# Kernel optimization log

Measured on AMD Instinct MI355X. Metric: run time of the kernel, lower is better.

The kernel has to match this reference:

```python
import jax, jax.numpy as jnp
import numpy as np

# irreps_in = 128x0e + 64x1o + 32x2e -> (multiplicity, 2l+1) blocks
IRREPS = [(128, 1), (64, 3), (32, 5)]
DIM = sum(m * d for m, d in IRREPS)  # 480
EPS = 1e-8


def setup_inputs() -> dict:
    key = jax.random.key(0)
    features = jax.random.normal(key, (100000, DIM), dtype=jnp.float32)
    return {"features": features}


def reference(features) -> jnp.ndarray:
    batch = features.shape[:-1]
    out_blocks = []
    off = 0
    for mul, d in IRREPS:  # fixed small structural loop over irrep types
        block = features[..., off:off + mul * d].reshape(*batch, mul, d)
        # per-irrep L2 norm over the (2l+1) components -> (..., mul)
        norms = jnp.sqrt(jnp.sum(block * block, axis=-1))
        eps_norms = jnp.maximum(norms, EPS)
        scalings = jax.nn.silu(eps_norms) / eps_norms
        out_blocks.append((block * scalings[..., None]).reshape(*batch, mul * d))
        off += mul * d
    return jnp.concatenate(out_blocks, axis=-1)
```

## Files before the change

kernel.cpp:

```cpp
#include <hip/hip_runtime.h>
#include <math.h>

#define DIM 480
#define ROWS 8
#define BLOCK 64
#define NLOADS 15

__device__ __forceinline__ float sig_of(float n) {
    n = fmaxf(n, 1e-8f);
    return __builtin_amdgcn_rcpf(1.0f + __expf(-n));
}

template <int R>
__device__ __forceinline__ void scale_groups(float* sbuf, int lane) {
    #pragma unroll
    for (int k = 0; k < R * 2; ++k) {
        const int a = k * 64 + lane;
        float* p = sbuf + (a >> 7) * DIM + (a & 127);
        const float x = *p;
        *p = x * sig_of(fabsf(x));
    }
    #pragma unroll
    for (int k = 0; k < R; ++k) {
        const int b = k * 64 + lane;
        float* p = sbuf + (b >> 6) * DIM + 128 + 3 * (b & 63);
        const float x0 = p[0], x1 = p[1], x2 = p[2];
        const float s = sig_of(sqrtf(x0*x0 + x1*x1 + x2*x2));
        p[0] = x0 * s; p[1] = x1 * s; p[2] = x2 * s;
    }
    #pragma unroll
    for (int k = 0; k < R / 2; ++k) {
        const int c = k * 64 + lane;
        float* p = sbuf + (c >> 5) * DIM + 320 + 5 * (c & 31);
        const float x0 = p[0], x1 = p[1], x2 = p[2], x3 = p[3], x4 = p[4];
        const float s = sig_of(sqrtf(x0*x0 + x1*x1 + x2*x2 + x3*x3 + x4*x4));
        p[0] = x0*s; p[1] = x1*s; p[2] = x2*s; p[3] = x3*s; p[4] = x4*s;
    }
}

__device__ void scale_groups_rt(float* sbuf, int lane, int rows) {
    for (int a = lane; a < rows * 128; a += 64) {
        float* p = sbuf + (a >> 7) * DIM + (a & 127);
        const float x = *p;
        *p = x * sig_of(fabsf(x));
    }
    for (int b = lane; b < rows * 64; b += 64) {
        float* p = sbuf + (b >> 6) * DIM + 128 + 3 * (b & 63);
        const float x0 = p[0], x1 = p[1], x2 = p[2];
        const float s = sig_of(sqrtf(x0*x0 + x1*x1 + x2*x2));
        p[0] = x0 * s; p[1] = x1 * s; p[2] = x2 * s;
    }
    for (int c = lane; c < rows * 32; c += 64) {
        float* p = sbuf + (c >> 5) * DIM + 320 + 5 * (c & 31);
        const float x0 = p[0], x1 = p[1], x2 = p[2], x3 = p[3], x4 = p[4];
        const float s = sig_of(sqrtf(x0*x0 + x1*x1 + x2*x2 + x3*x3 + x4*x4));
        p[0] = x0*s; p[1] = x1*s; p[2] = x2*s; p[3] = x3*s; p[4] = x4*s;
    }
}

__global__ __launch_bounds__(BLOCK) void norm_act_kernel(
    const float* __restrict__ in, float* __restrict__ out, int n_rows)
{
    __shared__ __align__(16) float sbuf[ROWS * DIM];
    const int lane = threadIdx.x;
    const int row0 = blockIdx.x * ROWS;
    const int rows = min(ROWS, n_rows - row0);

    const float* gsrc = in  + (size_t)row0 * DIM;
    float*       gdst = out + (size_t)row0 * DIM;

    if (rows == ROWS) {
        #pragma unroll
        for (int k = 0; k < NLOADS; ++k) {
            const float* gp = gsrc + (size_t)(k * 64 + lane) * 4;
            __builtin_amdgcn_global_load_lds(
                (const __attribute__((address_space(1))) void*)gp,
                (__attribute__((address_space(3))) void*)((char*)sbuf + k * 1024),
                16, 0, 0);
        }
        asm volatile("s_waitcnt vmcnt(0)" ::: "memory");

        scale_groups<ROWS>(sbuf, lane);

        #pragma unroll
        for (int k = 0; k < NLOADS; ++k) {
            const int v = k * 64 + lane;
            ((float4*)gdst)[v] = ((const float4*)sbuf)[v];
        }
    } else if (rows > 0) {
        for (int v = lane; v < rows * (DIM / 4); v += BLOCK)
            ((float4*)sbuf)[v] = ((const float4*)gsrc)[v];
        scale_groups_rt(sbuf, lane, rows);
        for (int v = lane; v < rows * (DIM / 4); v += BLOCK)
            ((float4*)gdst)[v] = ((const float4*)sbuf)[v];
    }
}

extern "C" void kernel_launch(void* const* d_in, const int* in_sizes, int n_in,
                              void* d_out, int out_size, void* d_ws, size_t ws_size,
                              hipStream_t stream) {
    const float* in  = (const float*)d_in[0];
    float*       out = (float*)d_out;
    const int n_rows = in_sizes[0] / DIM;
    const int grid   = (n_rows + ROWS - 1) / ROWS;
    norm_act_kernel<<<grid, BLOCK, 0, stream>>>(in, out, n_rows);
}
```

Measured before the change: 319.2 us.

## Make kernel persistent with double-buffered LDS prefetch of the next tile

Switches from one block per 8-row tile to a grid-stride persistent kernel capped at 1280 blocks. It double-buffers the LDS tile, issuing async global_load_lds for the next tile before processing the current one and waiting with a partial vmcnt. The goal is to overlap load latency with compute and stores within each wave and to reduce block launch overhead. In exchange it doubles LDS per block and cuts the number of resident waves, which may reduce memory-level parallelism.

```diff
diff --git a/kernel.cpp b/kernel.cpp
--- a/kernel.cpp
+++ b/kernel.cpp
@@ -5,6 +5,8 @@
 #define ROWS 8
 #define BLOCK 64
 #define NLOADS 15
+#define TILE_F (ROWS * DIM)
+#define NBLOCKS 1280
 
 __device__ __forceinline__ float sig_of(float n) {
     n = fmaxf(n, 1e-8f);
@@ -58,41 +60,63 @@
     }
 }
 
+__device__ __forceinline__ void stage_tile(const float* gsrc, float* dst, int lane) {
+    #pragma unroll
+    for (int k = 0; k < NLOADS; ++k) {
+        const float* gp = gsrc + (size_t)(k * 64 + lane) * 4;
+        __builtin_amdgcn_global_load_lds(
+            (const __attribute__((address_space(1))) void*)gp,
+            (__attribute__((address_space(3))) void*)((char*)dst + k * 1024),
+            16, 0, 0);
+    }
+}
+
 __global__ __launch_bounds__(BLOCK) void norm_act_kernel(
-    const float* __restrict__ in, float* __restrict__ out, int n_rows)
+    const float* __restrict__ in, float* __restrict__ out, int n_rows, int ntiles)
 {
-    __shared__ __align__(16) float sbuf[ROWS * DIM];
-    const int lane = threadIdx.x;
-    const int row0 = blockIdx.x * ROWS;
-    const int rows = min(ROWS, n_rows - row0);
+    __shared__ __align__(16) float sbuf[2 * TILE_F];
+    const int lane   = threadIdx.x;
+    const int stride = gridDim.x;
+    int t = blockIdx.x;
+    if (t >= ntiles) return;
 
-    const float* gsrc = in  + (size_t)row0 * DIM;
-    float*       gdst = out + (size_t)row0 * DIM;
+    int cur = 0;
+    if (t * ROWS + ROWS <= n_rows)
+        stage_tile(in + (size_t)t * TILE_F, sbuf, lane);
 
-    if (rows == ROWS) {
-        #pragma unroll
-        for (int k = 0; k < NLOADS; ++k) {
-            const float* gp = gsrc + (size_t)(k * 64 + lane) * 4;
-            __builtin_amdgcn_global_load_lds(
-                (const __attribute__((address_space(1))) void*)gp,
-                (__attribute__((address_space(3))) void*)((char*)sbuf + k * 1024),
-                16, 0, 0);
+    for (; t < ntiles; t += stride) {
+        const int row0 = t * ROWS;
+        const int rows = min(ROWS, n_rows - row0);
+        float* buf = sbuf + cur * TILE_F;
+
+        if (rows == ROWS) {
+            const int nt = t + stride;
+            if (nt < ntiles && nt * ROWS + ROWS <= n_rows) {
+                stage_tile(in + (size_t)nt * TILE_F, sbuf + (cur ^ 1) * TILE_F, lane);
+                asm volatile("s_waitcnt vmcnt(15)" ::: "memory");
+            } else {
+                asm volatile("s_waitcnt vmcnt(0)" ::: "memory");
+            }
+
+            scale_groups<ROWS>(buf, lane);
+
+            float* gdst = out + (size_t)row0 * DIM;
+            #pragma unroll
+            for (int k = 0; k < NLOADS; ++k) {
+                const int v = k * 64 + lane;
+                ((float4*)gdst)[v] = ((const float4*)buf)[v];
+            }
+        } else if (rows > 0) {
+            asm volatile("s_waitcnt vmcnt(0)" ::: "memory");
+            const float* gsrc = in + (size_t)row0 * DIM;
+            for (int v = lane; v < rows * (DIM / 4); v += BLOCK)
+                ((float4*)buf)[v] = ((const float4*)gsrc)[v];
+            scale_groups_rt(buf, lane, rows);
+            float* gdst = out + (size_t)row0 * DIM;
+            for (int v = lane; v < rows * (DIM / 4); v += BLOCK)
+                ((float4*)gdst)[v] = ((const float4*)buf)[v];
         }
-        asm volatile("s_waitcnt vmcnt(0)" ::: "memory");
-
-        scale_groups<ROWS>(sbuf, lane);
-
-        #pragma unroll
-        for (int k = 0; k < NLOADS; ++k) {
-            const int v = k * 64 + lane;
-            ((float4*)gdst)[v] = ((const float4*)sbuf)[v];
-        }
-    } else if (rows > 0) {
-        for (int v = lane; v < rows * (DIM / 4); v += BLOCK)
-            ((float4*)sbuf)[v] = ((const float4*)gsrc)[v];
-        scale_groups_rt(sbuf, lane, rows);
-        for (int v = lane; v < rows * (DIM / 4); v += BLOCK)
-            ((float4*)gdst)[v] = ((const float4*)sbuf)[v];
+        cur ^= 1;
     }
 }
 
@@ -102,6 +126,7 @@
     const float* in  = (const float*)d_in[0];
     float*       out = (float*)d_out;
     const int n_rows = in_sizes[0] / DIM;
-    const int grid   = (n_rows + ROWS - 1) / ROWS;
-    norm_act_kernel<<<grid, BLOCK, 0, stream>>>(in, out, n_rows);
+    const int ntiles = (n_rows + ROWS - 1) / ROWS;
+    const int grid   = ntiles < NBLOCKS ? ntiles : NBLOCKS;
+    norm_act_kernel<<<grid, BLOCK, 0, stream>>>(in, out, n_rows, ntiles);
 }
```

New measurement: 321.0 us. Within noise of the previous version (+0.5%).
